# Kernel tuning notes

Measured on AMD Instinct MI355X. Metric: run time of the kernel, lower is better.

## Reference

```python
import jax, jax.numpy as jnp
import numpy as np

N_NODES = 100000


def _gcn_conv(x, edge_index, W, b, n_nodes):
    # PyG GCNConv (default args): h = x @ W, add self-loops, symmetric
    # normalization D^-1/2 A_hat D^-1/2, aggregate sum, then + bias.
    row, col = edge_index[0], edge_index[1]          # source, target
    loop = jnp.arange(n_nodes, dtype=row.dtype)
    row = jnp.concatenate([row, loop])
    col = jnp.concatenate([col, loop])
    ew = jnp.ones(row.shape[0], dtype=x.dtype)       # edge_weight=None -> ones
    deg = jax.ops.segment_sum(ew, col, num_segments=n_nodes)
    dinv = jnp.where(deg > 0, jax.lax.rsqrt(deg), 0.0)
    norm = dinv[row] * ew * dinv[col]                # [E+N]
    h = x @ W                                        # [N, out]
    msg = h[row] * norm[:, None]                     # [E+N, out] gather
    out = jax.ops.segment_sum(msg, col, num_segments=n_nodes)  # scatter-add
    return out + b


def setup_inputs() -> dict:
    key = jax.random.key(0)
    k1, k2, k3, k4 = jax.random.split(key, 4)
    n, e, in_dim, hid, out = N_NODES, 1600000, 256, 128, 64
    x = jax.random.normal(k1, (n, in_dim), dtype=jnp.float32)
    edge_index = jax.random.randint(k2, (2, e), 0, n, dtype=jnp.int64)
    W1 = jax.random.normal(k3, (in_dim, hid), dtype=jnp.float32) / np.sqrt(in_dim)
    b1 = jnp.zeros((hid,), dtype=jnp.float32)
    W2 = jax.random.normal(k4, (hid, out), dtype=jnp.float32) / np.sqrt(hid)
    b2 = jnp.zeros((out,), dtype=jnp.float32)
    return {"x": x, "edge_index": edge_index, "W1": W1, "b1": b1, "W2": W2, "b2": b2}


def reference(x, edge_index, W1, b1, W2, b2):
    n = x.shape[0]
    h = _gcn_conv(x, edge_index, W1, b1, n)
    h = jax.nn.relu(h)
    # F.dropout with training=False (eval mode) is the identity.
    out = _gcn_conv(h, edge_index, W2, b2, n)
    return out
```

## Files before the change

kernel.cpp:

```cpp
#include <hip/hip_runtime.h>
#include <hip/hip_fp16.h>
#include <math.h>


typedef _Float16 f16;
typedef _Float16 f16x2 __attribute__((ext_vector_type(2)));
typedef _Float16 f16x4 __attribute__((ext_vector_type(4)));
typedef _Float16 f16x8 __attribute__((ext_vector_type(8)));
typedef float f32x4 __attribute__((ext_vector_type(4)));

#define CPAD 16

__global__ __launch_bounds__(256) void hist_rank(const int* __restrict__ ei, int E,
                                                 int* __restrict__ cnt,
                                                 int* __restrict__ rank, int N) {
  int base = (blockIdx.x * 256 + threadIdx.x) * 4;
  if (base + 4 <= E) {
    int4 c4 = *(const int4*)(ei + (size_t)E + base);
    int c[4] = {c4.x, c4.y, c4.z, c4.w};
    int r[4];
#pragma unroll
    for (int k = 0; k < 4; ++k)
      r[k] = ((unsigned)c[k] < (unsigned)N) ? atomicAdd(&cnt[(size_t)c[k] * CPAD], 1)
                                            : -1;
    int4 r4 = {r[0], r[1], r[2], r[3]};
    *(int4*)(rank + base) = r4;
  } else {
    for (int e = base; e < E; ++e) {
      int c = ei[(size_t)E + e];
      rank[e] = ((unsigned)c < (unsigned)N) ? atomicAdd(&cnt[(size_t)c * CPAD], 1) : -1;
    }
  }
}

__global__ __launch_bounds__(256) void scan_partial(const int* __restrict__ cnt,
                                                    int* __restrict__ offs,
                                                    int* __restrict__ bsums,
                                                    int N) {
  __shared__ int s[256];
  int t = threadIdx.x;
  int base = blockIdx.x * 1024 + t * 4;
  int v0 = (base + 0 < N) ? cnt[(size_t)(base + 0) * CPAD] : 0;
  int v1 = (base + 1 < N) ? cnt[(size_t)(base + 1) * CPAD] : 0;
  int v2 = (base + 2 < N) ? cnt[(size_t)(base + 2) * CPAD] : 0;
  int v3 = (base + 3 < N) ? cnt[(size_t)(base + 3) * CPAD] : 0;
  int sum = v0 + v1 + v2 + v3;
  s[t] = sum;
  __syncthreads();
#pragma unroll
  for (int d = 1; d < 256; d <<= 1) {
    int x = (t >= d) ? s[t - d] : 0;
    __syncthreads();
    s[t] += x;
    __syncthreads();
  }
  int excl = s[t] - sum;
  if (base + 0 < N) offs[base + 0] = excl;
  if (base + 1 < N) offs[base + 1] = excl + v0;
  if (base + 2 < N) offs[base + 2] = excl + v0 + v1;
  if (base + 3 < N) offs[base + 3] = excl + v0 + v1 + v2;
  if (t == 255) bsums[blockIdx.x] = s[255];
}

__global__ __launch_bounds__(256) void scan_bsums(int* __restrict__ bsums, int nb) {
  __shared__ int s[256];
  int t = threadIdx.x;
  int v = (t < nb) ? bsums[t] : 0;
  s[t] = v;
  __syncthreads();
#pragma unroll
  for (int d = 1; d < 256; d <<= 1) {
    int x = (t >= d) ? s[t - d] : 0;
    __syncthreads();
    s[t] += x;
    __syncthreads();
  }
  if (t < nb) bsums[t] = s[t] - v;
}

__global__ void finalize_kernel(const int* __restrict__ cnt, int* __restrict__ offs,
                                float* __restrict__ dinv,
                                const int* __restrict__ bsums, int N, int E) {
  int i = blockIdx.x * blockDim.x + threadIdx.x;
  if (i < N) {
    offs[i] += bsums[i >> 10];
    dinv[i] = 1.0f / sqrtf((float)cnt[(size_t)i * CPAD] + 1.0f);
    if (i == 0) offs[N] = E;
  }
}

__global__ __launch_bounds__(256) void fill_rank(const int* __restrict__ ei,
                                                 const int* __restrict__ rank,
                                                 const int* __restrict__ offs,
                                                 int E, int* __restrict__ csr, int N) {
  int base = (blockIdx.x * 256 + threadIdx.x) * 8;
  if (base + 8 <= E) {
    int4 s0 = *(const int4*)(ei + base);
    int4 s1 = *(const int4*)(ei + base + 4);
    int4 c0 = *(const int4*)(ei + (size_t)E + base);
    int4 c1 = *(const int4*)(ei + (size_t)E + base + 4);
    int4 r0 = *(const int4*)(rank + base);
    int4 r1 = *(const int4*)(rank + base + 4);
    int s[8] = {s0.x, s0.y, s0.z, s0.w, s1.x, s1.y, s1.z, s1.w};
    int c[8] = {c0.x, c0.y, c0.z, c0.w, c1.x, c1.y, c1.z, c1.w};
    int r[8] = {r0.x, r0.y, r0.z, r0.w, r1.x, r1.y, r1.z, r1.w};
#pragma unroll
    for (int k = 0; k < 8; ++k) {
      if (r[k] >= 0 && (unsigned)c[k] < (unsigned)N && (unsigned)s[k] < (unsigned)N)
        csr[offs[c[k]] + r[k]] = s[k];
    }
  } else {
    for (int e = base; e < E; ++e) {
      int s = ei[e], c = ei[(size_t)E + e], r = rank[e];
      if (r >= 0 && (unsigned)c < (unsigned)N && (unsigned)s < (unsigned)N)
        csr[offs[c] + r] = s;
    }
  }
}

__global__ void cvtT(const float* __restrict__ W, f16* __restrict__ Wt, int K, int N) {
  int i = blockIdx.x * 256 + threadIdx.x;
  if (i < K * N) {
    int k = i / N, n = i % N;
    Wt[(size_t)n * K + k] = (f16)W[i];
  }
}

template <int K, int NC, bool AHALF>
__global__ __launch_bounds__(256) void gemm_mfma(const void* __restrict__ Ain,
                                                 const f16* __restrict__ Bt,
                                                 const float* __restrict__ dinv,
                                                 f16* __restrict__ out, int M) {
  constexpr int BM = 128, BK = 64, LDR = BK + 8;
  constexpr int NF = NC / 16;
  __shared__ f16 als[BM][LDR];
  __shared__ f16 bls[NC][LDR];
  const int t = threadIdx.x;
  const int lane = t & 63, w = t >> 6;
  const int r0 = blockIdx.x * BM;

  f32x4 acc[2][NF];
#pragma unroll
  for (int fr = 0; fr < 2; ++fr)
#pragma unroll
    for (int fc = 0; fc < NF; ++fc) acc[fr][fc] = (f32x4){0.f, 0.f, 0.f, 0.f};

  for (int kt = 0; kt < K; kt += BK) {
    if constexpr (AHALF) {
      const f16* Ag = (const f16*)Ain;
#pragma unroll
      for (int i0 = 0; i0 < 4; ++i0) {
        int i = t + i0 * 256;
        int row = i >> 3, ko = i & 7;
        int gr = min(r0 + row, M - 1);
        f16x8 v = *(const f16x8*)(Ag + (size_t)gr * K + kt + ko * 8);
        *(f16x4*)&als[row][ko * 8] = __builtin_shufflevector(v, v, 0, 1, 2, 3);
        *(f16x4*)&als[row][ko * 8 + 4] = __builtin_shufflevector(v, v, 4, 5, 6, 7);
      }
    } else {
      const float* Ag = (const float*)Ain;
#pragma unroll
      for (int i0 = 0; i0 < 8; ++i0) {
        int i = t + i0 * 256;
        int row = i >> 4, kq = i & 15;
        int gr = min(r0 + row, M - 1);
        float4 v = *(const float4*)(Ag + (size_t)gr * K + kt + kq * 4);
        f16x4 h = {(f16)v.x, (f16)v.y, (f16)v.z, (f16)v.w};
        *(f16x4*)&als[row][kq * 4] = h;
      }
    }
#pragma unroll
    for (int i0 = 0; i0 < NC / 32; ++i0) {
      int i = t + i0 * 256;
      int n = i >> 3, ko = i & 7;
      f16x8 v = *(const f16x8*)(Bt + (size_t)n * K + kt + ko * 8);
      *(f16x4*)&bls[n][ko * 8] = __builtin_shufflevector(v, v, 0, 1, 2, 3);
      *(f16x4*)&bls[n][ko * 8 + 4] = __builtin_shufflevector(v, v, 4, 5, 6, 7);
    }
    __syncthreads();
#pragma unroll
    for (int ks = 0; ks < 2; ++ks) {
      int kb = ks * 32 + ((lane >> 4) << 3);
      f16x8 a[2];
#pragma unroll
      for (int fr = 0; fr < 2; ++fr) {
        f16x4 lo = *(const f16x4*)&als[w * 32 + fr * 16 + (lane & 15)][kb];
        f16x4 hi = *(const f16x4*)&als[w * 32 + fr * 16 + (lane & 15)][kb + 4];
        a[fr] = __builtin_shufflevector(lo, hi, 0, 1, 2, 3, 4, 5, 6, 7);
      }
#pragma unroll
      for (int fc = 0; fc < NF; ++fc) {
        f16x4 lo = *(const f16x4*)&bls[fc * 16 + (lane & 15)][kb];
        f16x4 hi = *(const f16x4*)&bls[fc * 16 + (lane & 15)][kb + 4];
        f16x8 b = __builtin_shufflevector(lo, hi, 0, 1, 2, 3, 4, 5, 6, 7);
#pragma unroll
        for (int fr = 0; fr < 2; ++fr)
          acc[fr][fc] =
              __builtin_amdgcn_mfma_f32_16x16x32_f16(a[fr], b, acc[fr][fc], 0, 0, 0);
      }
    }
    __syncthreads();
  }
#pragma unroll
  for (int fr = 0; fr < 2; ++fr) {
#pragma unroll
    for (int reg = 0; reg < 4; ++reg) {
      int row = r0 + w * 32 + fr * 16 + ((lane >> 4) << 2) + reg;
      if (row < M) {
        float s = dinv[row];
#pragma unroll
        for (int fc = 0; fc < NF; ++fc)
          out[(size_t)row * NC + fc * 16 + (lane & 15)] = (f16)(acc[fr][fc][reg] * s);
      }
    }
  }
}

__global__ __launch_bounds__(256) void aggregate1_f16(
    const f16* __restrict__ hs, const int* __restrict__ offs,
    const int* __restrict__ csr, const float* __restrict__ dinv,
    const float* __restrict__ bias, f16* __restrict__ out, int N) {
  int node = blockIdx.x * 4 + (threadIdx.x >> 6);
  if (node >= N) return;
  int lane = threadIdx.x & 63;
  int beg = __builtin_amdgcn_readfirstlane(offs[node]);
  int end = __builtin_amdgcn_readfirstlane(offs[node + 1]);
  float scale = dinv[node];
  f16x2 sv = *(const f16x2*)(hs + (size_t)node * 128 + lane * 2);
  float ax = (float)sv[0], ay = (float)sv[1];
  for (int j0 = beg; j0 < end; j0 += 64) {
    int cnt = min(64, end - j0);
    int myidx = 0;
    if (lane < cnt) myidx = csr[j0 + lane];
    int k = 0;
    for (; k + 8 <= cnt; k += 8) {
      f16x2 v[8];
#pragma unroll
      for (int u = 0; u < 8; ++u) {
        unsigned r = min((unsigned)__shfl(myidx, k + u), (unsigned)(N - 1));
        v[u] = *(const f16x2*)(hs + (size_t)r * 128 + lane * 2);
      }
#pragma unroll
      for (int u = 0; u < 8; ++u) {
        ax += (float)v[u][0];
        ay += (float)v[u][1];
      }
    }
    for (; k < cnt; ++k) {
      unsigned r = min((unsigned)__shfl(myidx, k), (unsigned)(N - 1));
      f16x2 v = *(const f16x2*)(hs + (size_t)r * 128 + lane * 2);
      ax += (float)v[0];
      ay += (float)v[1];
    }
  }
  float2 b = *(const float2*)(bias + lane * 2);
  float ox = fmaxf(fmaf(scale, ax, b.x), 0.f);
  float oy = fmaxf(fmaf(scale, ay, b.y), 0.f);
  f16x2 o = {(f16)ox, (f16)oy};
  *(f16x2*)(out + (size_t)node * 128 + lane * 2) = o;
}

__global__ __launch_bounds__(256) void aggregate2_f16(
    const f16* __restrict__ hs, const int* __restrict__ offs,
    const int* __restrict__ csr, const float* __restrict__ dinv,
    const float* __restrict__ bias, float* __restrict__ out, int N) {
  int node = blockIdx.x * 8 + (threadIdx.x >> 5);
  if (node >= N) return;
  int sl = threadIdx.x & 31;
  int beg = offs[node], end = offs[node + 1];
  float scale = dinv[node];
  f16x2 sv = *(const f16x2*)(hs + (size_t)node * 64 + sl * 2);
  float ax = (float)sv[0], ay = (float)sv[1];
  for (int j0 = beg; j0 < end; j0 += 32) {
    int cnt = min(32, end - j0);
    int myidx = 0;
    if (sl < cnt) myidx = csr[j0 + sl];
    int k = 0;
    for (; k + 8 <= cnt; k += 8) {
      f16x2 v[8];
#pragma unroll
      for (int u = 0; u < 8; ++u) {
        unsigned r = min((unsigned)__shfl(myidx, k + u, 32), (unsigned)(N - 1));
        v[u] = *(const f16x2*)(hs + (size_t)r * 64 + sl * 2);
      }
#pragma unroll
      for (int u = 0; u < 8; ++u) {
        ax += (float)v[u][0];
        ay += (float)v[u][1];
      }
    }
    for (; k < cnt; ++k) {
      unsigned r = min((unsigned)__shfl(myidx, k, 32), (unsigned)(N - 1));
      f16x2 v = *(const f16x2*)(hs + (size_t)r * 64 + sl * 2);
      ax += (float)v[0];
      ay += (float)v[1];
    }
  }
  float2 b = *(const float2*)(bias + sl * 2);
  float2 o = {fmaf(scale, ax, b.x), fmaf(scale, ay, b.y)};
  *(float2*)(out + (size_t)node * 64 + sl * 2) = o;
}

extern "C" void kernel_launch(void* const* d_in, const int* in_sizes, int n_in,
                              void* d_out, int out_size, void* d_ws, size_t ws_size,
                              hipStream_t stream) {
  const float* x = (const float*)d_in[0];
  const int* ei = (const int*)d_in[1];
  const float* W1 = (const float*)d_in[2];
  const float* b1 = (const float*)d_in[3];
  const float* W2 = (const float*)d_in[4];
  const float* b2 = (const float*)d_in[5];
  float* out = (float*)d_out;

  const int IN = 256, HID = 128, OUT = 64;
  int N = in_sizes[0] / IN;
  int E = in_sizes[1] / 2;

  char* ws = (char*)d_ws;
  size_t off = 0;
  auto alloc = [&](size_t bytes) -> void* {
    void* p = ws + off;
    off += (bytes + 255) & ~(size_t)255;
    return p;
  };
  int* cnt = (int*)alloc((size_t)N * CPAD * 4);
  int* offs = (int*)alloc(((size_t)N + 1) * 4);
  int* rank = (int*)alloc((size_t)E * 4);
  float* dinv = (float*)alloc((size_t)N * 4);
  int* bsums = (int*)alloc(1024 * 4);
  int* csr = (int*)alloc((size_t)E * 4);
  f16* Wt1 = (f16*)alloc((size_t)IN * HID * 2);
  f16* Wt2 = (f16*)alloc((size_t)HID * OUT * 2);
  f16* h1s = (f16*)alloc((size_t)N * HID * 2);
  f16* a1 = (f16*)alloc((size_t)N * HID * 2);
  f16* h2s = h1s;

  cvtT<<<(IN * HID + 255) / 256, 256, 0, stream>>>(W1, Wt1, IN, HID);
  cvtT<<<(HID * OUT + 255) / 256, 256, 0, stream>>>(W2, Wt2, HID, OUT);

  hipMemsetAsync(cnt, 0, (size_t)N * CPAD * 4, stream);
  int eb4 = (E / 4 + 255) / 256 + 1;
  hist_rank<<<eb4, 256, 0, stream>>>(ei, E, cnt, rank, N);
  int nb = (N + 1023) / 1024;
  scan_partial<<<nb, 256, 0, stream>>>(cnt, offs, bsums, N);
  scan_bsums<<<1, 256, 0, stream>>>(bsums, nb);
  finalize_kernel<<<(N + 255) / 256, 256, 0, stream>>>(cnt, offs, dinv, bsums, N, E);
  int eb8 = (E / 8 + 255) / 256 + 1;
  fill_rank<<<eb8, 256, 0, stream>>>(ei, rank, offs, E, csr, N);

  int gb = (N + 127) / 128;
  gemm_mfma<256, 128, false><<<gb, 256, 0, stream>>>(x, Wt1, dinv, h1s, N);
  aggregate1_f16<<<(N + 3) / 4, 256, 0, stream>>>(h1s, offs, csr, dinv, b1, a1, N);
  gemm_mfma<128, 64, true><<<gb, 256, 0, stream>>>(a1, Wt2, dinv, h2s, N);
  aggregate2_f16<<<(N + 7) / 8, 256, 0, stream>>>(h2s, offs, csr, dinv, b2, out, N);
}
```

Baseline: 398.5 us.

## Overlap atomic rank histogram with first GEMM in a fused launch

```diff
diff --git a/kernel.cpp b/kernel.cpp
--- a/kernel.cpp
+++ b/kernel.cpp
@@ -11,10 +11,28 @@
 
 #define CPAD 16
 
-__global__ __launch_bounds__(256) void hist_rank(const int* __restrict__ ei, int E,
-                                                 int* __restrict__ cnt,
-                                                 int* __restrict__ rank, int N) {
-  int base = (blockIdx.x * 256 + threadIdx.x) * 4;
+__global__ __launch_bounds__(256) void hist_fast(const int* __restrict__ ei, int E,
+                                                 int* __restrict__ cnt, int N) {
+  int base = (blockIdx.x * 256 + threadIdx.x) * 8;
+  if (base + 8 <= E) {
+    int4 c0 = *(const int4*)(ei + (size_t)E + base);
+    int4 c1 = *(const int4*)(ei + (size_t)E + base + 4);
+    int c[8] = {c0.x, c0.y, c0.z, c0.w, c1.x, c1.y, c1.z, c1.w};
+#pragma unroll
+    for (int k = 0; k < 8; ++k)
+      if ((unsigned)c[k] < (unsigned)N) atomicAdd(&cnt[c[k]], 1);
+  } else {
+    for (int e = base; e < E; ++e) {
+      int c = ei[(size_t)E + e];
+      if ((unsigned)c < (unsigned)N) atomicAdd(&cnt[c], 1);
+    }
+  }
+}
+
+__device__ __forceinline__ void hist_rank_body(int bid, const int* __restrict__ ei,
+                                               int E, int* __restrict__ cnt,
+                                               int* __restrict__ rank, int N) {
+  int base = (bid * 256 + (int)threadIdx.x) * 4;
   if (base + 4 <= E) {
     int4 c4 = *(const int4*)(ei + (size_t)E + base);
     int c[4] = {c4.x, c4.y, c4.z, c4.w};
@@ -40,10 +58,10 @@
   __shared__ int s[256];
   int t = threadIdx.x;
   int base = blockIdx.x * 1024 + t * 4;
-  int v0 = (base + 0 < N) ? cnt[(size_t)(base + 0) * CPAD] : 0;
-  int v1 = (base + 1 < N) ? cnt[(size_t)(base + 1) * CPAD] : 0;
-  int v2 = (base + 2 < N) ? cnt[(size_t)(base + 2) * CPAD] : 0;
-  int v3 = (base + 3 < N) ? cnt[(size_t)(base + 3) * CPAD] : 0;
+  int v0 = (base + 0 < N) ? cnt[base + 0] : 0;
+  int v1 = (base + 1 < N) ? cnt[base + 1] : 0;
+  int v2 = (base + 2 < N) ? cnt[base + 2] : 0;
+  int v3 = (base + 3 < N) ? cnt[base + 3] : 0;
   int sum = v0 + v1 + v2 + v3;
   s[t] = sum;
   __syncthreads();
@@ -84,7 +102,7 @@
   int i = blockIdx.x * blockDim.x + threadIdx.x;
   if (i < N) {
     offs[i] += bsums[i >> 10];
-    dinv[i] = 1.0f / sqrtf((float)cnt[(size_t)i * CPAD] + 1.0f);
+    dinv[i] = 1.0f / sqrtf((float)cnt[i] + 1.0f);
     if (i == 0) offs[N] = E;
   }
 }
@@ -127,17 +145,19 @@
 }
 
 template <int K, int NC, bool AHALF>
-__global__ __launch_bounds__(256) void gemm_mfma(const void* __restrict__ Ain,
-                                                 const f16* __restrict__ Bt,
-                                                 const float* __restrict__ dinv,
-                                                 f16* __restrict__ out, int M) {
+__device__ __forceinline__ void gemm_body(int bid, const void* __restrict__ Ain,
+                                          const f16* __restrict__ Bt,
+                                          const float* __restrict__ dinv,
+                                          f16* __restrict__ outp, int M,
+                                          f16* alsRaw, f16* blsRaw) {
   constexpr int BM = 128, BK = 64, LDR = BK + 8;
   constexpr int NF = NC / 16;
-  __shared__ f16 als[BM][LDR];
-  __shared__ f16 bls[NC][LDR];
+  typedef f16(*arr_t)[LDR];
+  arr_t als = (arr_t)alsRaw;
+  arr_t bls = (arr_t)blsRaw;
   const int t = threadIdx.x;
   const int lane = t & 63, w = t >> 6;
-  const int r0 = blockIdx.x * BM;
+  const int r0 = bid * BM;
 
   f32x4 acc[2][NF];
 #pragma unroll
@@ -210,10 +230,55 @@
         float s = dinv[row];
 #pragma unroll
         for (int fc = 0; fc < NF; ++fc)
-          out[(size_t)row * NC + fc * 16 + (lane & 15)] = (f16)(acc[fr][fc][reg] * s);
-      }
-    }
-  }
+          outp[(size_t)row * NC + fc * 16 + (lane & 15)] = (f16)(acc[fr][fc][reg] * s);
+      }
+    }
+  }
+}
+
+template <int K, int NC, bool AHALF>
+__global__ __launch_bounds__(256) void gemm_mfma(const void* __restrict__ Ain,
+                                                 const f16* __restrict__ Bt,
+                                                 const float* __restrict__ dinv,
+                                                 f16* __restrict__ out, int M) {
+  __shared__ f16 als[128 * 72];
+  __shared__ f16 bls[NC * 72];
+  gemm_body<K, NC, AHALF>(blockIdx.x, Ain, Bt, dinv, out, M, als, bls);
+}
+
+template <int K, int NC>
+__global__ __launch_bounds__(256) void fused_gemm1_hist(
+    const float* __restrict__ x, const f16* __restrict__ Bt,
+    const float* __restrict__ dinv, f16* __restrict__ h1, int M, int gb,
+    const int* __restrict__ ei, int E, int* __restrict__ cntB,
+    int* __restrict__ rank, int N, int histBlocks) {
+  __shared__ f16 als[128 * 72];
+  __shared__ f16 bls[NC * 72];
+  int bid = blockIdx.x;
+  bool isG;
+  int idx;
+  if (histBlocks == 2 * gb) {
+    int g = bid / 3;
+    if (bid % 3 == 2) {
+      isG = true;
+      idx = g;
+    } else {
+      isG = false;
+      idx = bid - g;
+    }
+  } else {
+    if (bid < histBlocks) {
+      isG = false;
+      idx = bid;
+    } else {
+      isG = true;
+      idx = bid - histBlocks;
+    }
+  }
+  if (isG)
+    gemm_body<K, NC, false>(idx, x, Bt, dinv, h1, M, als, bls);
+  else
+    hist_rank_body(idx, ei, E, cntB, rank, N);
 }
 
 __global__ __launch_bounds__(256) void aggregate1_f16(
@@ -323,7 +388,8 @@
     off += (bytes + 255) & ~(size_t)255;
     return p;
   };
-  int* cnt = (int*)alloc((size_t)N * CPAD * 4);
+  int* cntA = (int*)alloc((size_t)N * 4);
+  int* cntB = (int*)alloc((size_t)N * CPAD * 4);
   int* offs = (int*)alloc(((size_t)N + 1) * 4);
   int* rank = (int*)alloc((size_t)E * 4);
   float* dinv = (float*)alloc((size_t)N * 4);
@@ -338,18 +404,22 @@
   cvtT<<<(IN * HID + 255) / 256, 256, 0, stream>>>(W1, Wt1, IN, HID);
   cvtT<<<(HID * OUT + 255) / 256, 256, 0, stream>>>(W2, Wt2, HID, OUT);
 
-  hipMemsetAsync(cnt, 0, (size_t)N * CPAD * 4, stream);
+  hipMemsetAsync(cntA, 0, (size_t)N * 4, stream);
+  hipMemsetAsync(cntB, 0, (size_t)N * CPAD * 4, stream);
+
+  int eb8 = (E / 8 + 255) / 256 + 1;
+  hist_fast<<<eb8, 256, 0, stream>>>(ei, E, cntA, N);
+  int nb = (N + 1023) / 1024;
+  scan_partial<<<nb, 256, 0, stream>>>(cntA, offs, bsums, N);
+  scan_bsums<<<1, 256, 0, stream>>>(bsums, nb);
+  finalize_kernel<<<(N + 255) / 256, 256, 0, stream>>>(cntA, offs, dinv, bsums, N, E);
+
+  int gb = (N + 127) / 128;
   int eb4 = (E / 4 + 255) / 256 + 1;
-  hist_rank<<<eb4, 256, 0, stream>>>(ei, E, cnt, rank, N);
-  int nb = (N + 1023) / 1024;
-  scan_partial<<<nb, 256, 0, stream>>>(cnt, offs, bsums, N);
-  scan_bsums<<<1, 256, 0, stream>>>(bsums, nb);
-  finalize_kernel<<<(N + 255) / 256, 256, 0, stream>>>(cnt, offs, dinv, bsums, N, E);
-  int eb8 = (E / 8 + 255) / 256 + 1;
+  fused_gemm1_hist<256, 128><<<gb + eb4, 256, 0, stream>>>(
+      x, Wt1, dinv, h1s, N, gb, ei, E, cntB, rank, N, eb4);
+
   fill_rank<<<eb8, 256, 0, stream>>>(ei, rank, offs, E, csr, N);
-
-  int gb = (N + 127) / 128;
-  gemm_mfma<256, 128, false><<<gb, 256, 0, stream>>>(x, Wt1, dinv, h1s, N);
   aggregate1_f16<<<(N + 3) / 4, 256, 0, stream>>>(h1s, offs, csr, dinv, b1, a1, N);
   gemm_mfma<128, 64, true><<<gb, 256, 0, stream>>>(a1, Wt2, dinv, h2s, N);
   aggregate2_f16<<<(N + 7) / 8, 256, 0, stream>>>(h2s, offs, csr, dinv, b2, out, N);
```

Measured after the change: 452.9 us. 1.14x slower.

## Fuse first GEMM with histogram kernel to overlap compute and atomics

Applied to the files above, without the earlier changes.

```diff
diff --git a/kernel.cpp b/kernel.cpp
--- a/kernel.cpp
+++ b/kernel.cpp
@@ -11,24 +11,29 @@
 
 #define CPAD 16
 
-__global__ __launch_bounds__(256) void hist_rank(const int* __restrict__ ei, int E,
-                                                 int* __restrict__ cnt,
-                                                 int* __restrict__ rank, int N) {
-  int base = (blockIdx.x * 256 + threadIdx.x) * 4;
-  if (base + 4 <= E) {
-    int4 c4 = *(const int4*)(ei + (size_t)E + base);
-    int c[4] = {c4.x, c4.y, c4.z, c4.w};
-    int r[4];
-#pragma unroll
-    for (int k = 0; k < 4; ++k)
-      r[k] = ((unsigned)c[k] < (unsigned)N) ? atomicAdd(&cnt[(size_t)c[k] * CPAD], 1)
-                                            : -1;
-    int4 r4 = {r[0], r[1], r[2], r[3]};
-    *(int4*)(rank + base) = r4;
-  } else {
-    for (int e = base; e < E; ++e) {
-      int c = ei[(size_t)E + e];
-      rank[e] = ((unsigned)c < (unsigned)N) ? atomicAdd(&cnt[(size_t)c * CPAD], 1) : -1;
+__device__ __forceinline__ void hist_rank_body(int hb, int histBlocks,
+                                               const int* __restrict__ ei, int E,
+                                               int* __restrict__ cnt,
+                                               int* __restrict__ rank, int N) {
+  int stride = histBlocks * 256 * 4;
+  for (int base = (hb * 256 + (int)threadIdx.x) * 4; base < E; base += stride) {
+    if (base + 4 <= E) {
+      int4 c4 = *(const int4*)(ei + (size_t)E + base);
+      int c[4] = {c4.x, c4.y, c4.z, c4.w};
+      int r[4];
+#pragma unroll
+      for (int k = 0; k < 4; ++k)
+        r[k] = ((unsigned)c[k] < (unsigned)N)
+                   ? atomicAdd(&cnt[(size_t)c[k] * CPAD], 1)
+                   : -1;
+      int4 r4 = {r[0], r[1], r[2], r[3]};
+      *(int4*)(rank + base) = r4;
+    } else {
+      for (int e = base; e < E; ++e) {
+        int c = ei[(size_t)E + e];
+        rank[e] =
+            ((unsigned)c < (unsigned)N) ? atomicAdd(&cnt[(size_t)c * CPAD], 1) : -1;
+      }
     }
   }
 }
@@ -127,17 +132,19 @@
 }
 
 template <int K, int NC, bool AHALF>
-__global__ __launch_bounds__(256) void gemm_mfma(const void* __restrict__ Ain,
-                                                 const f16* __restrict__ Bt,
-                                                 const float* __restrict__ dinv,
-                                                 f16* __restrict__ out, int M) {
+__device__ __forceinline__ void gemm_body(int bid, const void* __restrict__ Ain,
+                                          const f16* __restrict__ Bt,
+                                          const float* __restrict__ dinv,
+                                          f16* __restrict__ outp, int M,
+                                          f16* alsRaw, f16* blsRaw) {
   constexpr int BM = 128, BK = 64, LDR = BK + 8;
   constexpr int NF = NC / 16;
-  __shared__ f16 als[BM][LDR];
-  __shared__ f16 bls[NC][LDR];
+  typedef f16(*arr_t)[LDR];
+  arr_t als = (arr_t)alsRaw;
+  arr_t bls = (arr_t)blsRaw;
   const int t = threadIdx.x;
   const int lane = t & 63, w = t >> 6;
-  const int r0 = blockIdx.x * BM;
+  const int r0 = bid * BM;
 
   f32x4 acc[2][NF];
 #pragma unroll
@@ -207,12 +214,37 @@
     for (int reg = 0; reg < 4; ++reg) {
       int row = r0 + w * 32 + fr * 16 + ((lane >> 4) << 2) + reg;
       if (row < M) {
-        float s = dinv[row];
+        float s = dinv ? dinv[row] : 1.0f;
 #pragma unroll
         for (int fc = 0; fc < NF; ++fc)
-          out[(size_t)row * NC + fc * 16 + (lane & 15)] = (f16)(acc[fr][fc][reg] * s);
-      }
-    }
+          outp[(size_t)row * NC + fc * 16 + (lane & 15)] = (f16)(acc[fr][fc][reg] * s);
+      }
+    }
+  }
+}
+
+template <int K, int NC, bool AHALF>
+__global__ __launch_bounds__(256) void gemm_mfma(const void* __restrict__ Ain,
+                                                 const f16* __restrict__ Bt,
+                                                 const float* __restrict__ dinv,
+                                                 f16* __restrict__ out, int M) {
+  __shared__ f16 als[128 * 72];
+  __shared__ f16 bls[NC * 72];
+  gemm_body<K, NC, AHALF>(blockIdx.x, Ain, Bt, dinv, out, M, als, bls);
+}
+
+template <int K, int NC>
+__global__ __launch_bounds__(256) void fused_gemm1_hist(
+    const float* __restrict__ x, const f16* __restrict__ Bt, f16* __restrict__ h1,
+    int M, const int* __restrict__ ei, int E, int* __restrict__ cntB,
+    int* __restrict__ rank, int N, int histBlocks) {
+  __shared__ f16 als[128 * 72];
+  __shared__ f16 bls[NC * 72];
+  int bid = blockIdx.x;
+  if (bid < histBlocks) {
+    hist_rank_body(bid, histBlocks, ei, E, cntB, rank, N);
+  } else {
+    gemm_body<K, NC, false>(bid - histBlocks, x, Bt, nullptr, h1, M, als, bls);
   }
 }
 
@@ -227,7 +259,7 @@
   int end = __builtin_amdgcn_readfirstlane(offs[node + 1]);
   float scale = dinv[node];
   f16x2 sv = *(const f16x2*)(hs + (size_t)node * 128 + lane * 2);
-  float ax = (float)sv[0], ay = (float)sv[1];
+  float ax = scale * (float)sv[0], ay = scale * (float)sv[1];
   for (int j0 = beg; j0 < end; j0 += 64) {
     int cnt = min(64, end - j0);
     int myidx = 0;
@@ -235,22 +267,25 @@
     int k = 0;
     for (; k + 8 <= cnt; k += 8) {
       f16x2 v[8];
+      float d[8];
 #pragma unroll
       for (int u = 0; u < 8; ++u) {
         unsigned r = min((unsigned)__shfl(myidx, k + u), (unsigned)(N - 1));
         v[u] = *(const f16x2*)(hs + (size_t)r * 128 + lane * 2);
+        d[u] = dinv[r];
       }
 #pragma unroll
       for (int u = 0; u < 8; ++u) {
-        ax += (float)v[u][0];
-        ay += (float)v[u][1];
+        ax = fmaf(d[u], (float)v[u][0], ax);
+        ay = fmaf(d[u], (float)v[u][1], ay);
       }
     }
     for (; k < cnt; ++k) {
       unsigned r = min((unsigned)__shfl(myidx, k), (unsigned)(N - 1));
       f16x2 v = *(const f16x2*)(hs + (size_t)r * 128 + lane * 2);
-      ax += (float)v[0];
-      ay += (float)v[1];
+      float d = dinv[r];
+      ax = fmaf(d, (float)v[0], ax);
+      ay = fmaf(d, (float)v[1], ay);
     }
   }
   float2 b = *(const float2*)(bias + lane * 2);
@@ -323,7 +358,7 @@
     off += (bytes + 255) & ~(size_t)255;
     return p;
   };
-  int* cnt = (int*)alloc((size_t)N * CPAD * 4);
+  int* cntB = (int*)alloc((size_t)N * CPAD * 4);
   int* offs = (int*)alloc(((size_t)N + 1) * 4);
   int* rank = (int*)alloc((size_t)E * 4);
   float* dinv = (float*)alloc((size_t)N * 4);
@@ -337,19 +372,20 @@
 
   cvtT<<<(IN * HID + 255) / 256, 256, 0, stream>>>(W1, Wt1, IN, HID);
   cvtT<<<(HID * OUT + 255) / 256, 256, 0, stream>>>(W2, Wt2, HID, OUT);
-
-  hipMemsetAsync(cnt, 0, (size_t)N * CPAD * 4, stream);
-  int eb4 = (E / 4 + 255) / 256 + 1;
-  hist_rank<<<eb4, 256, 0, stream>>>(ei, E, cnt, rank, N);
+  hipMemsetAsync(cntB, 0, (size_t)N * CPAD * 4, stream);
+
+  int gb = (N + 127) / 128;
+  const int histBlocks = 256;
+  fused_gemm1_hist<256, 128><<<histBlocks + gb, 256, 0, stream>>>(
+      x, Wt1, h1s, N, ei, E, cntB, rank, N, histBlocks);
+
   int nb = (N + 1023) / 1024;
-  scan_partial<<<nb, 256, 0, stream>>>(cnt, offs, bsums, N);
+  scan_partial<<<nb, 256, 0, stream>>>(cntB, offs, bsums, N);
   scan_bsums<<<1, 256, 0, stream>>>(bsums, nb);
-  finalize_kernel<<<(N + 255) / 256, 256, 0, stream>>>(cnt, offs, dinv, bsums, N, E);
+  finalize_kernel<<<(N + 255) / 256, 256, 0, stream>>>(cntB, offs, dinv, bsums, N, E);
+
   int eb8 = (E / 8 + 255) / 256 + 1;
   fill_rank<<<eb8, 256, 0, stream>>>(ei, rank, offs, E, csr, N);
-
-  int gb = (N + 127) / 128;
-  gemm_mfma<256, 128, false><<<gb, 256, 0, stream>>>(x, Wt1, dinv, h1s, N);
   aggregate1_f16<<<(N + 3) / 4, 256, 0, stream>>>(h1s, offs, csr, dinv, b1, a1, N);
   gemm_mfma<128, 64, true><<<gb, 256, 0, stream>>>(a1, Wt2, dinv, h2s, N);
   aggregate2_f16<<<(N + 7) / 8, 256, 0, stream>>>(h2s, offs, csr, dinv, b2, out, N);
```

Measured after the change: 389.2 us. 1.02x faster.

## Build CSR with two-level bucket sort using LDS atomics instead of global atomics

Applied to the files above, without the earlier changes.

```diff
diff --git a/kernel.cpp b/kernel.cpp
--- a/kernel.cpp
+++ b/kernel.cpp
@@ -9,42 +9,35 @@
 typedef _Float16 f16x8 __attribute__((ext_vector_type(8)));
 typedef float f32x4 __attribute__((ext_vector_type(4)));
 
-#define CPAD 16
-
-__global__ __launch_bounds__(256) void hist_rank(const int* __restrict__ ei, int E,
-                                                 int* __restrict__ cnt,
-                                                 int* __restrict__ rank, int N) {
-  int base = (blockIdx.x * 256 + threadIdx.x) * 4;
-  if (base + 4 <= E) {
-    int4 c4 = *(const int4*)(ei + (size_t)E + base);
-    int c[4] = {c4.x, c4.y, c4.z, c4.w};
-    int r[4];
-#pragma unroll
-    for (int k = 0; k < 4; ++k)
-      r[k] = ((unsigned)c[k] < (unsigned)N) ? atomicAdd(&cnt[(size_t)c[k] * CPAD], 1)
-                                            : -1;
-    int4 r4 = {r[0], r[1], r[2], r[3]};
-    *(int4*)(rank + base) = r4;
-  } else {
-    for (int e = base; e < E; ++e) {
-      int c = ei[(size_t)E + e];
-      rank[e] = ((unsigned)c < (unsigned)N) ? atomicAdd(&cnt[(size_t)c * CPAD], 1) : -1;
-    }
-  }
-}
-
-__global__ __launch_bounds__(256) void scan_partial(const int* __restrict__ cnt,
-                                                    int* __restrict__ offs,
-                                                    int* __restrict__ bsums,
-                                                    int N) {
+#define NBLK1 1024
+#define NPB 512
+#define NBMAX 256
+
+__global__ __launch_bounds__(256) void pass1_count(const int* __restrict__ ei, int E,
+                                                   int* __restrict__ cntmat, int N,
+                                                   int NB, int EPB) {
+  __shared__ int bcnt[NBMAX];
+  int t = threadIdx.x;
+  for (int j = t; j < NB; j += 256) bcnt[j] = 0;
+  __syncthreads();
+  int beg = blockIdx.x * EPB, end = min(E, beg + EPB);
+  for (int e = beg + t; e < end; e += 256) {
+    int c = ei[(size_t)E + e];
+    if ((unsigned)c < (unsigned)N) atomicAdd(&bcnt[c >> 9], 1);
+  }
+  __syncthreads();
+  for (int j = t; j < NB; j += 256) cntmat[(size_t)blockIdx.x * NB + j] = bcnt[j];
+}
+
+__global__ __launch_bounds__(256) void scan_cntmat(const int* __restrict__ cntmat,
+                                                   int* __restrict__ basemat,
+                                                   int* __restrict__ bsums2, int NB) {
   __shared__ int s[256];
-  int t = threadIdx.x;
-  int base = blockIdx.x * 1024 + t * 4;
-  int v0 = (base + 0 < N) ? cnt[(size_t)(base + 0) * CPAD] : 0;
-  int v1 = (base + 1 < N) ? cnt[(size_t)(base + 1) * CPAD] : 0;
-  int v2 = (base + 2 < N) ? cnt[(size_t)(base + 2) * CPAD] : 0;
-  int v3 = (base + 3 < N) ? cnt[(size_t)(base + 3) * CPAD] : 0;
-  int sum = v0 + v1 + v2 + v3;
+  int t = threadIdx.x, g = blockIdx.x;
+  int v[4];
+#pragma unroll
+  for (int u = 0; u < 4; ++u) v[u] = cntmat[(size_t)(t * 4 + u) * NB + g];
+  int sum = v[0] + v[1] + v[2] + v[3];
   s[t] = sum;
   __syncthreads();
 #pragma unroll
@@ -55,11 +48,14 @@
     __syncthreads();
   }
   int excl = s[t] - sum;
-  if (base + 0 < N) offs[base + 0] = excl;
-  if (base + 1 < N) offs[base + 1] = excl + v0;
-  if (base + 2 < N) offs[base + 2] = excl + v0 + v1;
-  if (base + 3 < N) offs[base + 3] = excl + v0 + v1 + v2;
-  if (t == 255) bsums[blockIdx.x] = s[255];
+  int o = excl;
+  int* bm = basemat + (size_t)g * NBLK1 + t * 4;
+#pragma unroll
+  for (int u = 0; u < 4; ++u) {
+    bm[u] = o;
+    o += v[u];
+  }
+  if (t == 255) bsums2[g] = s[255];
 }
 
 __global__ __launch_bounds__(256) void scan_bsums(int* __restrict__ bsums, int nb) {
@@ -78,42 +74,81 @@
   if (t < nb) bsums[t] = s[t] - v;
 }
 
-__global__ void finalize_kernel(const int* __restrict__ cnt, int* __restrict__ offs,
-                                float* __restrict__ dinv,
-                                const int* __restrict__ bsums, int N, int E) {
-  int i = blockIdx.x * blockDim.x + threadIdx.x;
-  if (i < N) {
-    offs[i] += bsums[i >> 10];
-    dinv[i] = 1.0f / sqrtf((float)cnt[(size_t)i * CPAD] + 1.0f);
-    if (i == 0) offs[N] = E;
-  }
-}
-
-__global__ __launch_bounds__(256) void fill_rank(const int* __restrict__ ei,
-                                                 const int* __restrict__ rank,
-                                                 const int* __restrict__ offs,
-                                                 int E, int* __restrict__ csr, int N) {
-  int base = (blockIdx.x * 256 + threadIdx.x) * 8;
-  if (base + 8 <= E) {
-    int4 s0 = *(const int4*)(ei + base);
-    int4 s1 = *(const int4*)(ei + base + 4);
-    int4 c0 = *(const int4*)(ei + (size_t)E + base);
-    int4 c1 = *(const int4*)(ei + (size_t)E + base + 4);
-    int4 r0 = *(const int4*)(rank + base);
-    int4 r1 = *(const int4*)(rank + base + 4);
-    int s[8] = {s0.x, s0.y, s0.z, s0.w, s1.x, s1.y, s1.z, s1.w};
-    int c[8] = {c0.x, c0.y, c0.z, c0.w, c1.x, c1.y, c1.z, c1.w};
-    int r[8] = {r0.x, r0.y, r0.z, r0.w, r1.x, r1.y, r1.z, r1.w};
-#pragma unroll
-    for (int k = 0; k < 8; ++k) {
-      if (r[k] >= 0 && (unsigned)c[k] < (unsigned)N && (unsigned)s[k] < (unsigned)N)
-        csr[offs[c[k]] + r[k]] = s[k];
-    }
-  } else {
-    for (int e = base; e < E; ++e) {
-      int s = ei[e], c = ei[(size_t)E + e], r = rank[e];
-      if (r >= 0 && (unsigned)c < (unsigned)N && (unsigned)s < (unsigned)N)
-        csr[offs[c] + r] = s;
+__global__ __launch_bounds__(256) void pass2_scatter(const int* __restrict__ ei, int E,
+                                                     const int* __restrict__ basemat,
+                                                     const int* __restrict__ bsums2,
+                                                     int2* __restrict__ bucket_arr,
+                                                     int N, int NB, int EPB) {
+  __shared__ int curs[NBMAX];
+  int t = threadIdx.x, bid = blockIdx.x;
+  for (int j = t; j < NB; j += 256)
+    curs[j] = basemat[(size_t)j * NBLK1 + bid] + bsums2[j];
+  __syncthreads();
+  int beg = bid * EPB, end = min(E, beg + EPB);
+  for (int e = beg + t; e < end; e += 256) {
+    int c = ei[(size_t)E + e];
+    if ((unsigned)c < (unsigned)N) {
+      int srcv = ei[e];
+      int pos = atomicAdd(&curs[c >> 9], 1);
+      bucket_arr[pos] = make_int2(srcv, c);
+    }
+  }
+}
+
+__global__ __launch_bounds__(256) void pass3_build(const int2* __restrict__ bucket_arr,
+                                                   const int* __restrict__ basemat,
+                                                   const int* __restrict__ bsums2,
+                                                   int* __restrict__ offs,
+                                                   float* __restrict__ dinv,
+                                                   int* __restrict__ csr, int E, int N,
+                                                   int NB) {
+  __shared__ int cnt[NPB];
+  __shared__ int curs[NPB];
+  __shared__ int s[256];
+  int t = threadIdx.x, b = blockIdx.x;
+  int lo = b * NPB;
+  cnt[t] = 0;
+  cnt[t + 256] = 0;
+  __syncthreads();
+  int beg = basemat[(size_t)b * NBLK1] + bsums2[b];
+  int end = (b + 1 < NB) ? (basemat[(size_t)(b + 1) * NBLK1] + bsums2[b + 1]) : E;
+  for (int e = beg + t; e < end; e += 256) {
+    int2 sc = bucket_arr[e];
+    unsigned idx = (unsigned)(sc.y - lo);
+    if (idx < NPB) atomicAdd(&cnt[idx], 1);
+  }
+  __syncthreads();
+  int v0 = cnt[2 * t], v1 = cnt[2 * t + 1];
+  int sum = v0 + v1;
+  s[t] = sum;
+  __syncthreads();
+#pragma unroll
+  for (int d = 1; d < 256; d <<= 1) {
+    int x = (t >= d) ? s[t - d] : 0;
+    __syncthreads();
+    s[t] += x;
+    __syncthreads();
+  }
+  int excl = s[t] - sum;
+  int o0 = beg + excl, o1 = beg + excl + v0;
+  curs[2 * t] = o0;
+  curs[2 * t + 1] = o1;
+  if (lo + 2 * t < N) {
+    offs[lo + 2 * t] = o0;
+    dinv[lo + 2 * t] = 1.0f / sqrtf((float)v0 + 1.0f);
+  }
+  if (lo + 2 * t + 1 < N) {
+    offs[lo + 2 * t + 1] = o1;
+    dinv[lo + 2 * t + 1] = 1.0f / sqrtf((float)v1 + 1.0f);
+  }
+  if (b == NB - 1 && t == 0) offs[N] = E;
+  __syncthreads();
+  for (int e = beg + t; e < end; e += 256) {
+    int2 sc = bucket_arr[e];
+    unsigned idx = (unsigned)(sc.y - lo);
+    if (idx < NPB) {
+      int pos = atomicAdd(&curs[idx], 1);
+      csr[pos] = sc.x;
     }
   }
 }
@@ -130,7 +165,7 @@
 __global__ __launch_bounds__(256) void gemm_mfma(const void* __restrict__ Ain,
                                                  const f16* __restrict__ Bt,
                                                  const float* __restrict__ dinv,
-                                                 f16* __restrict__ out, int M) {
+                                                 f16* __restrict__ outp, int M) {
   constexpr int BM = 128, BK = 64, LDR = BK + 8;
   constexpr int NF = NC / 16;
   __shared__ f16 als[BM][LDR];
@@ -207,10 +242,10 @@
     for (int reg = 0; reg < 4; ++reg) {
       int row = r0 + w * 32 + fr * 16 + ((lane >> 4) << 2) + reg;
       if (row < M) {
-        float s = dinv[row];
+        float sc = dinv ? dinv[row] : 1.0f;
 #pragma unroll
         for (int fc = 0; fc < NF; ++fc)
-          out[(size_t)row * NC + fc * 16 + (lane & 15)] = (f16)(acc[fr][fc][reg] * s);
+          outp[(size_t)row * NC + fc * 16 + (lane & 15)] = (f16)(acc[fr][fc][reg] * sc);
       }
     }
   }
@@ -227,7 +262,7 @@
   int end = __builtin_amdgcn_readfirstlane(offs[node + 1]);
   float scale = dinv[node];
   f16x2 sv = *(const f16x2*)(hs + (size_t)node * 128 + lane * 2);
-  float ax = (float)sv[0], ay = (float)sv[1];
+  float ax = scale * (float)sv[0], ay = scale * (float)sv[1];
   for (int j0 = beg; j0 < end; j0 += 64) {
     int cnt = min(64, end - j0);
     int myidx = 0;
@@ -235,22 +270,25 @@
     int k = 0;
     for (; k + 8 <= cnt; k += 8) {
       f16x2 v[8];
+      float d[8];
 #pragma unroll
       for (int u = 0; u < 8; ++u) {
         unsigned r = min((unsigned)__shfl(myidx, k + u), (unsigned)(N - 1));
         v[u] = *(const f16x2*)(hs + (size_t)r * 128 + lane * 2);
+        d[u] = dinv[r];
       }
 #pragma unroll
       for (int u = 0; u < 8; ++u) {
-        ax += (float)v[u][0];
-        ay += (float)v[u][1];
+        ax = fmaf(d[u], (float)v[u][0], ax);
+        ay = fmaf(d[u], (float)v[u][1], ay);
       }
     }
     for (; k < cnt; ++k) {
       unsigned r = min((unsigned)__shfl(myidx, k), (unsigned)(N - 1));
       f16x2 v = *(const f16x2*)(hs + (size_t)r * 128 + lane * 2);
-      ax += (float)v[0];
-      ay += (float)v[1];
+      float d = dinv[r];
+      ax = fmaf(d, (float)v[0], ax);
+      ay = fmaf(d, (float)v[1], ay);
     }
   }
   float2 b = *(const float2*)(bias + lane * 2);
@@ -315,6 +353,8 @@
   const int IN = 256, HID = 128, OUT = 64;
   int N = in_sizes[0] / IN;
   int E = in_sizes[1] / 2;
+  int NB = (N + NPB - 1) / NPB;
+  int EPB = (E + NBLK1 - 1) / NBLK1;
 
   char* ws = (char*)d_ws;
   size_t off = 0;
@@ -323,11 +363,12 @@
     off += (bytes + 255) & ~(size_t)255;
     return p;
   };
-  int* cnt = (int*)alloc((size_t)N * CPAD * 4);
+  int* cntmat = (int*)alloc((size_t)NBLK1 * NB * 4);
+  int* basemat = (int*)alloc((size_t)NB * NBLK1 * 4);
+  int* bsums2 = (int*)alloc(1024 * 4);
+  int2* bucket_arr = (int2*)alloc((size_t)E * 8);
   int* offs = (int*)alloc(((size_t)N + 1) * 4);
-  int* rank = (int*)alloc((size_t)E * 4);
   float* dinv = (float*)alloc((size_t)N * 4);
-  int* bsums = (int*)alloc(1024 * 4);
   int* csr = (int*)alloc((size_t)E * 4);
   f16* Wt1 = (f16*)alloc((size_t)IN * HID * 2);
   f16* Wt2 = (f16*)alloc((size_t)HID * OUT * 2);
@@ -338,18 +379,17 @@
   cvtT<<<(IN * HID + 255) / 256, 256, 0, stream>>>(W1, Wt1, IN, HID);
   cvtT<<<(HID * OUT + 255) / 256, 256, 0, stream>>>(W2, Wt2, HID, OUT);
 
-  hipMemsetAsync(cnt, 0, (size_t)N * CPAD * 4, stream);
-  int eb4 = (E / 4 + 255) / 256 + 1;
-  hist_rank<<<eb4, 256, 0, stream>>>(ei, E, cnt, rank, N);
-  int nb = (N + 1023) / 1024;
-  scan_partial<<<nb, 256, 0, stream>>>(cnt, offs, bsums, N);
-  scan_bsums<<<1, 256, 0, stream>>>(bsums, nb);
-  finalize_kernel<<<(N + 255) / 256, 256, 0, stream>>>(cnt, offs, dinv, bsums, N, E);
-  int eb8 = (E / 8 + 255) / 256 + 1;
-  fill_rank<<<eb8, 256, 0, stream>>>(ei, rank, offs, E, csr, N);
-
   int gb = (N + 127) / 128;
-  gemm_mfma<256, 128, false><<<gb, 256, 0, stream>>>(x, Wt1, dinv, h1s, N);
+  gemm_mfma<256, 128, false><<<gb, 256, 0, stream>>>(x, Wt1, nullptr, h1s, N);
+
+  pass1_count<<<NBLK1, 256, 0, stream>>>(ei, E, cntmat, N, NB, EPB);
+  scan_cntmat<<<NB, 256, 0, stream>>>(cntmat, basemat, bsums2, NB);
+  scan_bsums<<<1, 256, 0, stream>>>(bsums2, NB);
+  pass2_scatter<<<NBLK1, 256, 0, stream>>>(ei, E, basemat, bsums2, bucket_arr, N, NB,
+                                           EPB);
+  pass3_build<<<NB, 256, 0, stream>>>(bucket_arr, basemat, bsums2, offs, dinv, csr, E,
+                                      N, NB);
+
   aggregate1_f16<<<(N + 3) / 4, 256, 0, stream>>>(h1s, offs, csr, dinv, b1, a1, N);
   gemm_mfma<128, 64, true><<<gb, 256, 0, stream>>>(a1, Wt2, dinv, h2s, N);
   aggregate2_f16<<<(N + 7) / 8, 256, 0, stream>>>(h2s, offs, csr, dinv, b2, out, N);
```

Result: faster. 381.4 us (-4.3%).
